# Performance work log

Measured on AMD Instinct MI355X. Metric: run time of the kernel, lower is better.

Reference implementation:

```python
import jax, jax.numpy as jnp
import numpy as np

N_NODES = 50000; N_EDGES = 600000; N_GRAPHS = 128
IN_CH = 128; PROJ = 128; OUT_CH = 128; K = 3; NCLASS = 2; EPS = 1e-5


def _mask():
    # xhi_layer_mask: block i (rows i*OUT_CH:(i+1)*OUT_CH) sees first PROJ*(i+1) input cols
    blocks = []
    for i in range(K):
        m = np.zeros((OUT_CH, PROJ * K), np.float32)
        m[:, :PROJ * (i + 1)] = 1.0
        blocks.append(m)
    return jnp.asarray(np.concatenate(blocks, 0))


def _bn(x, g, b):
    # BatchNorm1d in training mode: biased batch stats, affine g/b
    m = jnp.mean(x, axis=0)
    v = jnp.var(x, axis=0)
    return (x - m) * jax.lax.rsqrt(v + EPS) * g + b


def setup_inputs() -> dict:
    key = jax.random.key(0)
    ks = jax.random.split(key, 10)
    M = OUT_CH * K
    def w(k, shape):
        return jax.random.normal(k, shape, jnp.float32) * 0.05
    return {
        "x": jax.random.normal(ks[0], (N_NODES, IN_CH), jnp.float32),
        "edge_index": jax.random.randint(ks[1], (2, N_EDGES), 0, N_NODES),
        "batch": jnp.sort(jax.random.randint(ks[2], (N_NODES,), 0, N_GRAPHS)),
        "n_graphs": N_GRAPHS,
        "w_rel": w(ks[3], (PROJ, IN_CH)), "b_rel": jnp.zeros((PROJ,), jnp.float32),
        "w_root": w(ks[4], (PROJ, IN_CH)),
        "norm0_g": jnp.ones((PROJ,), jnp.float32), "norm0_b": jnp.zeros((PROJ,), jnp.float32),
        "lin_w": w(ks[5], (M, PROJ * K)), "lin_b": jnp.zeros((M,), jnp.float32),
        "bnh_g": jnp.ones((M,), jnp.float32), "bnh_b": jnp.zeros((M,), jnp.float32),
        "bno_g": jnp.ones((3 * M,), jnp.float32), "bno_b": jnp.zeros((3 * M,), jnp.float32),
        "w1": w(ks[6], (2 * M, 3 * M)), "b1": jnp.zeros((2 * M,), jnp.float32),
        "w2": w(ks[7], (M, 2 * M)), "b2": jnp.zeros((M,), jnp.float32),
        "w3": w(ks[8], (NCLASS, M)), "b3": jnp.zeros((NCLASS,), jnp.float32),
    }


def reference(x, edge_index, batch, n_graphs, w_rel, b_rel, w_root, norm0_g, norm0_b,
              lin_w, lin_b, bnh_g, bnh_b, bno_g, bno_b, w1, b1, w2, b2, w3, b3):
    row, col = edge_index[0], edge_index[1]
    # GraphConv: lin_rel(sum_{j->i} x_j) + lin_root(x_i)
    neigh = jax.ops.segment_sum(x[row], col, num_segments=N_NODES)
    X = neigh @ w_rel.T + b_rel + x @ w_root.T
    X = _bn(X, norm0_g, norm0_b)
    # k-hop polynomial diffusion: A^i X computed as iterative SpMM over edges
    # (A[r,c] = 1 for edge (r,c): (A v)[r] = sum over edges of v[c])
    H = [X]
    cur = X
    for _ in range(K - 1):
        cur = jax.ops.segment_sum(cur[col], row, num_segments=N_NODES)
        H.append(cur)
    Hc = jnp.concatenate(H, axis=1)  # [N, PROJ*K]
    Hm = _bn(Hc @ (lin_w * _mask()).T + lin_b, bnh_g, bnh_b)  # [N, OUT_CH*K]
    # global mean / add / max pooling per graph
    ones = jnp.ones((N_NODES,), jnp.float32)
    cnt = jax.ops.segment_sum(ones, batch, num_segments=n_graphs)
    Hadd = jax.ops.segment_sum(Hm, batch, num_segments=n_graphs)
    Havg = Hadd / jnp.maximum(cnt, 1.0)[:, None]
    Hmax = jax.ops.segment_max(Hm, batch, num_segments=n_graphs)
    Hmax = jnp.where(jnp.isfinite(Hmax), Hmax, 0.0)  # guard empty segments
    Hcat = jnp.concatenate([Havg, Hadd, Hmax], axis=1)  # [G, 3*OUT_CH*K]
    # funnel readout (dropout = identity in eval)
    h = _bn(Hcat, bno_g, bno_b)
    h = jax.nn.relu(h @ w1.T + b1)
    h = jax.nn.relu(h @ w2.T + b2)
    return jax.nn.log_softmax(h @ w3.T + b3, axis=1)
```

## Files before the change

### kernel.cpp

```cpp
#include <hip/hip_runtime.h>
#include <math.h>

#define N_NODES 50000
#define N_EDGES 600000
#define N_GRAPHS 128
#define IN_CH 128
#define PROJ 128
#define OUT_CH 128
#define M_DIM 384
#define HC_DIM 384
#define CAT_DIM 1152
#define H1_DIM 768
#define EPS 1e-5f
#define SCAN_BLK 256
#define NPART 8
#define PART_NODES 6250
#define NPB 64
#define NROWB 391

using bf16x8 = __attribute__((ext_vector_type(8))) short;
using f32x4  = __attribute__((ext_vector_type(4))) float;

__device__ inline unsigned short f2bf(float f) {
  unsigned u = __float_as_uint(f);
  unsigned r = u + 0x7fffu + ((u >> 16) & 1u);
  return (unsigned short)(r >> 16);
}
__device__ inline float bf2f(unsigned short h) {
  return __uint_as_float(((unsigned)h) << 16);
}

__device__ inline void atomicMaxF(float* addr, float val) {
  int iv = __float_as_int(val);
  if (iv >= 0) atomicMax((int*)addr, iv);
  else         atomicMin((unsigned int*)addr, (unsigned int)iv);
}
__device__ inline void atomicMinF(float* addr, float val) {
  int iv = __float_as_int(val);
  if (iv >= 0) atomicMin((int*)addr, iv);
  else         atomicMax((unsigned int*)addr, (unsigned int)iv);
}

__device__ inline void gld16(const void* g, void* l) {
  __builtin_amdgcn_global_load_lds(
      (const __attribute__((address_space(1))) void*)g,
      (__attribute__((address_space(3))) void*)l, 16, 0, 0);
}

__global__ void fill_minmax_kernel(float* __restrict__ gmax, float* __restrict__ gmin) {
  int i = blockIdx.x * blockDim.x + threadIdx.x;
  if (i < N_GRAPHS * M_DIM) {
    gmax[i] = -__builtin_inff();
    gmin[i] =  __builtin_inff();
  }
}

__global__ void bounds_kernel(const int* __restrict__ batch, int* __restrict__ start) {
  int i = blockIdx.x * blockDim.x + threadIdx.x;
  if (i >= N_NODES) return;
  int b = batch[i];
  int bp = (i == 0) ? -1 : batch[i - 1];
  for (int g = bp + 1; g <= b; ++g) start[g] = i;
  if (i == N_NODES - 1)
    for (int g = b + 1; g <= N_GRAPHS; ++g) start[g] = N_NODES;
}

__global__ void cnt_from_bounds_kernel(const int* __restrict__ start, float* __restrict__ cnt) {
  int g = threadIdx.x;
  if (g < N_GRAPHS) cnt[g] = (float)(start[g + 1] - start[g]);
}

__global__ __launch_bounds__(256) void hist_part_kernel(
    const int* __restrict__ row, const int* __restrict__ col,
    int* __restrict__ degA, int* __restrict__ degB) {
  const int part = blockIdx.x & (NPART - 1);
  const int slice = blockIdx.x >> 3;
  const int lo = part * PART_NODES, hi = lo + PART_NODES;
  for (int e = slice * 256 + threadIdx.x; e < N_EDGES; e += NPB * 256) {
    int r = row[e], c = col[e];
    if (c >= lo && c < hi) atomicAdd(&degA[c], 1);
    if (r >= lo && r < hi) atomicAdd(&degB[r], 1);
  }
}

__global__ __launch_bounds__(256) void fill_csr_part_kernel(
    const int* __restrict__ row, const int* __restrict__ col,
    int* __restrict__ cursA, int* __restrict__ eidxA,
    int* __restrict__ cursB, int* __restrict__ eidxB) {
  const int part = blockIdx.x & (NPART - 1);
  const int slice = blockIdx.x >> 3;
  const int lo = part * PART_NODES, hi = lo + PART_NODES;
  for (int e = slice * 256 + threadIdx.x; e < N_EDGES; e += NPB * 256) {
    int r = row[e], c = col[e];
    if (c >= lo && c < hi) eidxA[atomicAdd(&cursA[c], 1)] = r;
    if (r >= lo && r < hi) eidxB[atomicAdd(&cursB[r], 1)] = c;
  }
}

__global__ void scan1_kernel(const int* __restrict__ deg, int* __restrict__ offs,
                             int* __restrict__ bsum, int n) {
  __shared__ int sh[SCAN_BLK];
  int i = blockIdx.x * SCAN_BLK + threadIdx.x;
  int v = (i < n) ? deg[i] : 0;
  sh[threadIdx.x] = v; __syncthreads();
  #pragma unroll
  for (int d = 1; d < SCAN_BLK; d <<= 1) {
    int t = (threadIdx.x >= d) ? sh[threadIdx.x - d] : 0;
    __syncthreads();
    sh[threadIdx.x] += t;
    __syncthreads();
  }
  if (i < n) offs[i] = sh[threadIdx.x] - v;
  if (threadIdx.x == SCAN_BLK - 1) bsum[blockIdx.x] = sh[threadIdx.x];
}

__global__ void scan2_kernel(int* __restrict__ bsum, int nb) {
  __shared__ int sh[SCAN_BLK];
  int v = (threadIdx.x < nb) ? bsum[threadIdx.x] : 0;
  sh[threadIdx.x] = v; __syncthreads();
  #pragma unroll
  for (int d = 1; d < SCAN_BLK; d <<= 1) {
    int t = (threadIdx.x >= d) ? sh[threadIdx.x - d] : 0;
    __syncthreads();
    sh[threadIdx.x] += t;
    __syncthreads();
  }
  if (threadIdx.x < nb) bsum[threadIdx.x] = sh[threadIdx.x] - v;
}

__global__ void scan3_kernel(int* __restrict__ offs, const int* __restrict__ bsum,
                             int* __restrict__ cursor, int n) {
  int i = blockIdx.x * SCAN_BLK + threadIdx.x;
  if (i < n) {
    int o = offs[i] + bsum[blockIdx.x];
    offs[i] = o;
    cursor[i] = o;
  }
}

__global__ void convert_x_kernel(const float* __restrict__ x, unsigned short* __restrict__ xnb) {
  int t = blockIdx.x * blockDim.x + threadIdx.x;
  if (t >= N_NODES * 32) return;
  int node = t >> 5;
  int c4 = (t & 31) << 2;
  float4 v = *(const float4*)(x + (size_t)node * IN_CH + c4);
  ushort4 h = {f2bf(v.x), f2bf(v.y), f2bf(v.z), f2bf(v.w)};
  *(ushort4*)(xnb + (size_t)node * 256 + 128 + c4) = h;
}

__global__ void convert_wcat_kernel(const float* __restrict__ w_rel, const float* __restrict__ w_root,
                                    unsigned short* __restrict__ wcatb) {
  int t = blockIdx.x * blockDim.x + threadIdx.x;
  if (t >= 128 * 64) return;
  int n = t >> 6;
  int c4 = (t & 63) << 2;
  const float* src = (c4 < 128) ? (w_rel + (size_t)n * 128 + c4)
                                : (w_root + (size_t)n * 128 + (c4 - 128));
  float4 v = *(const float4*)src;
  ushort4 h = {f2bf(v.x), f2bf(v.y), f2bf(v.z), f2bf(v.w)};
  *(ushort4*)(wcatb + (size_t)n * 256 + c4) = h;
}

__global__ void convert_linw_kernel(const float* __restrict__ lin_w, unsigned short* __restrict__ linwb) {
  int t = blockIdx.x * blockDim.x + threadIdx.x;
  if (t >= 384 * 96) return;
  int n = t / 96;
  int c4 = (t - n * 96) << 2;
  float4 v = *(const float4*)(lin_w + (size_t)n * HC_DIM + c4);
  ushort4 h = {f2bf(v.x), f2bf(v.y), f2bf(v.z), f2bf(v.w)};
  *(ushort4*)(linwb + (size_t)n * HC_DIM + c4) = h;
}

__global__ __launch_bounds__(256) void gather_bf16_kernel(
    const unsigned short* __restrict__ src, const int* __restrict__ offs,
    const int* __restrict__ ends, const int* __restrict__ eidx,
    unsigned short* __restrict__ dst, int src_ld, int dst_ld) {
  int tid = blockIdx.x * blockDim.x + threadIdx.x;
  int node = tid >> 5;
  int c = (tid & 31) << 2;
  if (node >= N_NODES) return;
  int j = offs[node], end = ends[node];
  float ax = 0.f, ay = 0.f, az = 0.f, aw = 0.f;
  for (; j + 1 < end; j += 2) {
    int s0 = eidx[j], s1 = eidx[j + 1];
    ushort4 v0 = *(const ushort4*)(src + (size_t)s0 * src_ld + c);
    ushort4 v1 = *(const ushort4*)(src + (size_t)s1 * src_ld + c);
    ax += bf2f(v0.x); ay += bf2f(v0.y); az += bf2f(v0.z); aw += bf2f(v0.w);
    ax += bf2f(v1.x); ay += bf2f(v1.y); az += bf2f(v1.z); aw += bf2f(v1.w);
  }
  if (j < end) {
    int s0 = eidx[j];
    ushort4 v0 = *(const ushort4*)(src + (size_t)s0 * src_ld + c);
    ax += bf2f(v0.x); ay += bf2f(v0.y); az += bf2f(v0.z); aw += bf2f(v0.w);
  }
  ushort4 h = {f2bf(ax), f2bf(ay), f2bf(az), f2bf(aw)};
  *(ushort4*)(dst + (size_t)node * dst_ld + c) = h;
}

__device__ inline void stage_async(const unsigned short* __restrict__ src, int src_ld,
                                   int row0, int k0, char* __restrict__ zone, int t) {
  #pragma unroll
  for (int p = 0; p < 4; ++p) {
    int idx = p * 256 + t;
    int r = idx >> 3;
    int slot = idx & 7;
    int sslot = slot ^ (r & 7);
    const char* g = (const char*)(src + (size_t)(row0 + r) * src_ld + k0) + (sslot << 4);
    void* l = zone + p * 4096 + (t >> 6) * 1024;
    gld16(g, l);
  }
}

__device__ inline bf16x8 frag_ld(const char* __restrict__ zone, int row, int slot) {
  return *(const bf16x8*)(zone + row * 128 + ((slot ^ (row & 7)) << 4));
}

__global__ __launch_bounds__(256) void gemm_conv_mfma(
    const unsigned short* __restrict__ xnb, const unsigned short* __restrict__ wcatb,
    const float* __restrict__ b_rel, float* __restrict__ Hc0,
    float* __restrict__ colsum8, float* __restrict__ colsq8) {
  __shared__ char smem[32768];
  char* zoneA = smem;
  char* zoneB = smem + 16384;
  const int bm = blockIdx.x * 128;
  const int t = threadIdx.x;
  const int l = t & 63;
  const int wid = t >> 6;
  const int wr = wid >> 1, wc = wid & 1;
  const int lrow = l & 15, lk = l >> 4;
  f32x4 acc[4][4];
  #pragma unroll
  for (int i = 0; i < 4; ++i)
    #pragma unroll
    for (int jn = 0; jn < 4; ++jn) acc[i][jn] = (f32x4){0.f, 0.f, 0.f, 0.f};
  for (int st = 0; st < 4; ++st) {
    __syncthreads();
    stage_async(xnb, 256, bm, st * 64, zoneA, t);
    stage_async(wcatb, 256, 0, st * 64, zoneB, t);
    __syncthreads();
    #pragma unroll
    for (int kk = 0; kk < 2; ++kk) {
      bf16x8 af[4], bfr[4];
      #pragma unroll
      for (int mf = 0; mf < 4; ++mf) af[mf] = frag_ld(zoneA, wr * 64 + mf * 16 + lrow, kk * 4 + lk);
      #pragma unroll
      for (int nf = 0; nf < 4; ++nf) bfr[nf] = frag_ld(zoneB, wc * 64 + nf * 16 + lrow, kk * 4 + lk);
      #pragma unroll
      for (int mf = 0; mf < 4; ++mf)
        #pragma unroll
        for (int nf = 0; nf < 4; ++nf)
          acc[mf][nf] = __builtin_amdgcn_mfma_f32_16x16x32_bf16(af[mf], bfr[nf], acc[mf][nf], 0, 0, 0);
    }
  }
  float brv[4];
  #pragma unroll
  for (int nf = 0; nf < 4; ++nf) brv[nf] = b_rel[wc * 64 + nf * 16 + lrow];
  #pragma unroll
  for (int mf = 0; mf < 4; ++mf) {
    #pragma unroll
    for (int q = 0; q < 4; ++q) {
      int r = bm + wr * 64 + mf * 16 + lk * 4 + q;
      if (r < N_NODES) {
        #pragma unroll
        for (int nf = 0; nf < 4; ++nf)
          Hc0[(size_t)r * 128 + wc * 64 + nf * 16 + lrow] = acc[mf][nf][q] + brv[nf];
      }
    }
  }
  __syncthreads();
  float* csum = (float*)smem;
  float* csq  = (float*)(smem + 512);
  if (t < 128) { csum[t] = 0.f; csq[t] = 0.f; }
  __syncthreads();
  #pragma unroll
  for (int nf = 0; nf < 4; ++nf) {
    int ccol = wc * 64 + nf * 16 + lrow;
    float s = 0.f, q = 0.f;
    #pragma unroll
    for (int mf = 0; mf < 4; ++mf)
      #pragma unroll
      for (int qq = 0; qq < 4; ++qq) {
        int r = bm + wr * 64 + mf * 16 + lk * 4 + qq;
        if (r < N_NODES) { float v = acc[mf][nf][qq] + brv[nf]; s += v; q += v * v; }
      }
    atomicAdd(&csum[ccol], s);
    atomicAdd(&csq[ccol], q);
  }
  __syncthreads();
  if (t < 128) {
    int cpy = (blockIdx.x & 7) * 128;
    atomicAdd(&colsum8[cpy + t], csum[t]);
    atomicAdd(&colsq8[cpy + t], csq[t]);
  }
}

__global__ void bn_prep_kernel(const float* __restrict__ colsum8, const float* __restrict__ colsq8,
                               const float* __restrict__ g_, const float* __restrict__ b_,
                               float* __restrict__ bn_s, float* __restrict__ bn_t) {
  int c = threadIdx.x;
  float s1 = 0.f, s2 = 0.f;
  #pragma unroll
  for (int k = 0; k < 8; ++k) { s1 += colsum8[k * 128 + c]; s2 += colsq8[k * 128 + c]; }
  float m = s1 * (1.0f / N_NODES);
  float var = s2 * (1.0f / N_NODES) - m * m;
  float sc = g_[c] * rsqrtf(var + EPS);
  bn_s[c] = sc;
  bn_t[c] = b_[c] - m * sc;
}

__global__ __launch_bounds__(256) void gemm_mask_mfma(
    const unsigned short* __restrict__ Hcb, const unsigned short* __restrict__ linwb,
    const float* __restrict__ lin_b, const int* __restrict__ batch,
    float* __restrict__ gsum, float* __restrict__ gmax, float* __restrict__ gmin,
    float* __restrict__ colsumsq) {
  __shared__ char smem[33792];
  __shared__ int bsh[128];
  char* zoneA = smem;
  char* zoneB = smem + 16384;
  const int bid = blockIdx.x;
  const int ybl = 2 - bid / NROWB;
  const int bm = (bid % NROWB) * 128;
  const int bn = ybl * 128;
  const int nstages = 2 * (ybl + 1);
  const int t = threadIdx.x;
  const int l = t & 63;
  const int wid = t >> 6;
  const int wr = wid >> 1, wc = wid & 1;
  const int lrow = l & 15, lk = l >> 4;
  f32x4 acc[4][4];
  #pragma unroll
  for (int i = 0; i < 4; ++i)
    #pragma unroll
    for (int jn = 0; jn < 4; ++jn) acc[i][jn] = (f32x4){0.f, 0.f, 0.f, 0.f};
  for (int st = 0; st < nstages; ++st) {
    __syncthreads();
    stage_async(Hcb, HC_DIM, bm, st * 64, zoneA, t);
    stage_async(linwb, HC_DIM, bn, st * 64, zoneB, t);
    __syncthreads();
    #pragma unroll
    for (int kk = 0; kk < 2; ++kk) {
      bf16x8 af[4], bfr[4];
      #pragma unroll
      for (int mf = 0; mf < 4; ++mf) af[mf] = frag_ld(zoneA, wr * 64 + mf * 16 + lrow, kk * 4 + lk);
      #pragma unroll
      for (int nf = 0; nf < 4; ++nf) bfr[nf] = frag_ld(zoneB, wc * 64 + nf * 16 + lrow, kk * 4 + lk);
      #pragma unroll
      for (int mf = 0; mf < 4; ++mf)
        #pragma unroll
        for (int nf = 0; nf < 4; ++nf)
          acc[mf][nf] = __builtin_amdgcn_mfma_f32_16x16x32_bf16(af[mf], bfr[nf], acc[mf][nf], 0, 0, 0);
    }
  }
  float lbv[4];
  #pragma unroll
  for (int nf = 0; nf < 4; ++nf) lbv[nf] = lin_b[bn + wc * 64 + nf * 16 + lrow];
  if (t < 128) bsh[t] = (bm + t < N_NODES) ? batch[bm + t] : -1;
  float* Y = (float*)smem;
  const int col = t & 127;
  const int gcol = bn + col;
  const int r0 = (t >> 7) * 32;
  float sq = 0.f;
  __syncthreads();
  for (int half = 0; half < 2; ++half) {
    if (wr == half) {
      #pragma unroll
      for (int mf = 0; mf < 4; ++mf)
        #pragma unroll
        for (int q = 0; q < 4; ++q) {
          int rr = mf * 16 + lk * 4 + q;
          #pragma unroll
          for (int nf = 0; nf < 4; ++nf)
            Y[rr * 132 + wc * 64 + nf * 16 + lrow] = acc[mf][nf][q] + lbv[nf];
        }
    }
    __syncthreads();
    int curg = -1;
    float s = 0.f, mx = 0.f, mn = 0.f;
    for (int rr = 0; rr < 32; ++rr) {
      int g = bsh[half * 64 + r0 + rr];
      if (g < 0) break;
      float y = Y[(r0 + rr) * 132 + col];
      sq += y * y;
      if (g != curg) {
        if (curg >= 0) {
          atomicAdd(&gsum[curg * M_DIM + gcol], s);
          atomicMaxF(&gmax[curg * M_DIM + gcol], mx);
          atomicMinF(&gmin[curg * M_DIM + gcol], mn);
        }
        curg = g; s = y; mx = y; mn = y;
      } else {
        s += y; mx = fmaxf(mx, y); mn = fminf(mn, y);
      }
    }
    if (curg >= 0) {
      atomicAdd(&gsum[curg * M_DIM + gcol], s);
      atomicMaxF(&gmax[curg * M_DIM + gcol], mx);
      atomicMinF(&gmin[curg * M_DIM + gcol], mn);
    }
    __syncthreads();
  }
  atomicAdd(&colsumsq[gcol], sq);
}

__global__ __launch_bounds__(256) void bn_apply0_kernel(
    const float* __restrict__ Hc0, unsigned short* __restrict__ Hcb,
    const float* __restrict__ bn_s, const float* __restrict__ bn_t) {
  int tid = blockIdx.x * blockDim.x + threadIdx.x;
  if (tid >= N_NODES * 32) return;
  int r = tid >> 5;
  int c = (tid & 31) << 2;
  float4 v = *(const float4*)(Hc0 + (size_t)r * 128 + c);
  float vv[4] = {v.x, v.y, v.z, v.w};
  #pragma unroll
  for (int j = 0; j < 4; ++j)
    vv[j] = vv[j] * bn_s[c + j] + bn_t[c + j];
  ushort4 hh = {f2bf(vv[0]), f2bf(vv[1]), f2bf(vv[2]), f2bf(vv[3])};
  *(ushort4*)(Hcb + (size_t)r * HC_DIM + c) = hh;
}

__device__ inline float block_sum128(float v, float* red) {
  int t = threadIdx.x;
  red[t] = v; __syncthreads();
  #pragma unroll
  for (int s = 64; s >= 1; s >>= 1) {
    if (t < s) red[t] += red[t + s];
    __syncthreads();
  }
  float r = red[0];
  __syncthreads();
  return r;
}

__device__ inline void bn_write_col(float v, int col, const float* __restrict__ bg,
                                    const float* __restrict__ bb, float* __restrict__ h0T,
                                    float* red) {
  float s1 = block_sum128(v, red);
  float s2 = block_sum128(v * v, red);
  float m = s1 * (1.0f / N_GRAPHS);
  float var = s2 * (1.0f / N_GRAPHS) - m * m;
  float sc = bg[col] * rsqrtf(var + EPS);
  h0T[(size_t)col * N_GRAPHS + threadIdx.x] = (v - m) * sc + bb[col];
}

__global__ __launch_bounds__(128) void finalize_kernel(
    const float* __restrict__ gsum, const float* __restrict__ gmax,
    const float* __restrict__ gmin, const float* __restrict__ colsumsq,
    const float* __restrict__ cnt, const float* __restrict__ bnh_g,
    const float* __restrict__ bnh_b, const float* __restrict__ bno_g,
    const float* __restrict__ bno_b, float* __restrict__ h0T) {
  __shared__ float red[128];
  int c = blockIdx.x;
  int g = threadIdx.x;
  float vsum = gsum[g * M_DIM + c];
  float colsum = block_sum128(vsum, red);
  float m = colsum * (1.0f / N_NODES);
  float var = colsumsq[c] * (1.0f / N_NODES) - m * m;
  float s = bnh_g[c] * rsqrtf(var + EPS);
  float t = bnh_b[c] - m * s;
  float cg = cnt[g];
  float hadd = s * vsum + cg * t;
  float havg = hadd / fmaxf(cg, 1.0f);
  float hmax = 0.f;
  if (cg > 0.f)
    hmax = (s >= 0.f ? s * gmax[g * M_DIM + c] : s * gmin[g * M_DIM + c]) + t;
  bn_write_col(havg, c,        bno_g, bno_b, h0T, red);
  bn_write_col(hadd, 384 + c,  bno_g, bno_b, h0T, red);
  bn_write_col(hmax, 768 + c,  bno_g, bno_b, h0T, red);
}

__global__ __launch_bounds__(128) void mlp_kernel(
    const float* __restrict__ inT, const float* __restrict__ W,
    const float* __restrict__ bias, float* __restrict__ outT, int Kdim, int do_relu) {
  __shared__ float wrow[CAT_DIM];
  int oc = blockIdx.x;
  int g = threadIdx.x;
  for (int k = g; k < Kdim; k += 128) wrow[k] = W[(size_t)oc * Kdim + k];
  __syncthreads();
  float acc = bias[oc];
  for (int k = 0; k < Kdim; ++k) acc += inT[(size_t)k * N_GRAPHS + g] * wrow[k];
  if (do_relu) acc = fmaxf(acc, 0.f);
  outT[(size_t)oc * N_GRAPHS + g] = acc;
}

__global__ __launch_bounds__(128) void head_kernel(
    const float* __restrict__ h2T, const float* __restrict__ w3,
    const float* __restrict__ b3, float* __restrict__ out) {
  int g = threadIdx.x;
  float z0 = b3[0], z1 = b3[1];
  for (int k = 0; k < M_DIM; ++k) {
    float v = h2T[(size_t)k * N_GRAPHS + g];
    z0 += v * w3[k];
    z1 += v * w3[M_DIM + k];
  }
  float mz = fmaxf(z0, z1);
  float lse = mz + logf(expf(z0 - mz) + expf(z1 - mz));
  out[g * 2 + 0] = z0 - lse;
  out[g * 2 + 1] = z1 - lse;
}

extern "C" void kernel_launch(void* const* d_in, const int* in_sizes, int n_in,
                              void* d_out, int out_size, void* d_ws, size_t ws_size,
                              hipStream_t stream) {
  const float* x       = (const float*)d_in[0];
  const int*   row     = (const int*)d_in[1];
  const int*   col     = row + N_EDGES;
  const int*   batch   = (const int*)d_in[2];
  const float* w_rel   = (const float*)d_in[4];
  const float* b_rel   = (const float*)d_in[5];
  const float* w_root  = (const float*)d_in[6];
  const float* norm0_g = (const float*)d_in[7];
  const float* norm0_b = (const float*)d_in[8];
  const float* lin_w   = (const float*)d_in[9];
  const float* lin_b   = (const float*)d_in[10];
  const float* bnh_g   = (const float*)d_in[11];
  const float* bnh_b   = (const float*)d_in[12];
  const float* bno_g   = (const float*)d_in[13];
  const float* bno_b   = (const float*)d_in[14];
  const float* w1      = (const float*)d_in[15];
  const float* b1      = (const float*)d_in[16];
  const float* w2      = (const float*)d_in[17];
  const float* b2      = (const float*)d_in[18];
  const float* w3      = (const float*)d_in[19];
  const float* b3      = (const float*)d_in[20];
  float* out = (float*)d_out;

  char* ws = (char*)d_ws;
  size_t off = 0;
  auto allocb = [&](size_t nbytes) {
    char* p = ws + off;
    off += ((nbytes + 255) & ~(size_t)255);
    return p;
  };
  int*   degA      = (int*)allocb(N_NODES * 4);
  int*   degB      = (int*)allocb(N_NODES * 4);
  float* gsum      = (float*)allocb((size_t)N_GRAPHS * M_DIM * 4);
  float* colsumsq  = (float*)allocb(M_DIM * 4);
  float* colsum8   = (float*)allocb(8 * PROJ * 4);
  float* colsq8    = (float*)allocb(8 * PROJ * 4);
  size_t zero_bytes = off;
  float* cnt    = (float*)allocb(N_GRAPHS * 4);
  int*   gstart = (int*)allocb((N_GRAPHS + 1) * 4);
  float* bn_s   = (float*)allocb(PROJ * 4);
  float* bn_t   = (float*)allocb(PROJ * 4);
  int*   offsA = (int*)allocb(N_NODES * 4);
  int*   cursA = (int*)allocb(N_NODES * 4);
  int*   offsB = (int*)allocb(N_NODES * 4);
  int*   cursB = (int*)allocb(N_NODES * 4);
  int*   bsumA = (int*)allocb(SCAN_BLK * 4);
  int*   bsumB = (int*)allocb(SCAN_BLK * 4);
  int*   eidxA = (int*)allocb(N_EDGES * 4);
  int*   eidxB = (int*)allocb(N_EDGES * 4);
  float* Hc0   = (float*)allocb((size_t)N_NODES * 128 * 4);
  unsigned short* Hcb   = (unsigned short*)allocb((size_t)N_NODES * HC_DIM * 2);
  unsigned short* xnb   = (unsigned short*)allocb((size_t)N_NODES * 256 * 2);
  unsigned short* wcatb = (unsigned short*)allocb(128 * 256 * 2);
  unsigned short* linwb = (unsigned short*)allocb(384 * 384 * 2);
  float* gmax  = (float*)allocb((size_t)N_GRAPHS * M_DIM * 4);
  float* gmin  = (float*)allocb((size_t)N_GRAPHS * M_DIM * 4);
  float* h0T   = (float*)allocb((size_t)CAT_DIM * N_GRAPHS * 4);
  float* h1T   = (float*)allocb((size_t)H1_DIM * N_GRAPHS * 4);
  float* h2T   = (float*)allocb((size_t)M_DIM * N_GRAPHS * 4);

  const int NB = (N_NODES + SCAN_BLK - 1) / SCAN_BLK;

  hipMemsetAsync(d_ws, 0, zero_bytes, stream);
  fill_minmax_kernel<<<(N_GRAPHS * M_DIM + 255) / 256, 256, 0, stream>>>(gmax, gmin);
  bounds_kernel<<<(N_NODES + 255) / 256, 256, 0, stream>>>(batch, gstart);
  cnt_from_bounds_kernel<<<1, 128, 0, stream>>>(gstart, cnt);

  hist_part_kernel<<<NPART * NPB, 256, 0, stream>>>(row, col, degA, degB);
  scan1_kernel<<<NB, SCAN_BLK, 0, stream>>>(degA, offsA, bsumA, N_NODES);
  scan1_kernel<<<NB, SCAN_BLK, 0, stream>>>(degB, offsB, bsumB, N_NODES);
  scan2_kernel<<<1, SCAN_BLK, 0, stream>>>(bsumA, NB);
  scan2_kernel<<<1, SCAN_BLK, 0, stream>>>(bsumB, NB);
  scan3_kernel<<<NB, SCAN_BLK, 0, stream>>>(offsA, bsumA, cursA, N_NODES);
  scan3_kernel<<<NB, SCAN_BLK, 0, stream>>>(offsB, bsumB, cursB, N_NODES);
  fill_csr_part_kernel<<<NPART * NPB, 256, 0, stream>>>(row, col, cursA, eidxA, cursB, eidxB);

  convert_x_kernel<<<(N_NODES * 32 + 255) / 256, 256, 0, stream>>>(x, xnb);
  convert_wcat_kernel<<<(128 * 64 + 255) / 256, 256, 0, stream>>>(w_rel, w_root, wcatb);
  convert_linw_kernel<<<(384 * 96 + 255) / 256, 256, 0, stream>>>(lin_w, linwb);

  gather_bf16_kernel<<<(N_NODES * 32 + 255) / 256, 256, 0, stream>>>(
      xnb + 128, offsA, cursA, eidxA, xnb, 256, 256);
  gemm_conv_mfma<<<NROWB, 256, 0, stream>>>(xnb, wcatb, b_rel, Hc0, colsum8, colsq8);
  bn_prep_kernel<<<1, 128, 0, stream>>>(colsum8, colsq8, norm0_g, norm0_b, bn_s, bn_t);
  bn_apply0_kernel<<<(N_NODES * 32 + 255) / 256, 256, 0, stream>>>(Hc0, Hcb, bn_s, bn_t);
  gather_bf16_kernel<<<(N_NODES * 32 + 255) / 256, 256, 0, stream>>>(
      Hcb, offsB, cursB, eidxB, Hcb + 128, HC_DIM, HC_DIM);
  gather_bf16_kernel<<<(N_NODES * 32 + 255) / 256, 256, 0, stream>>>(
      Hcb + 128, offsB, cursB, eidxB, Hcb + 256, HC_DIM, HC_DIM);
  gemm_mask_mfma<<<NROWB * 3, 256, 0, stream>>>(
      Hcb, linwb, lin_b, batch, gsum, gmax, gmin, colsumsq);
  finalize_kernel<<<M_DIM, 128, 0, stream>>>(gsum, gmax, gmin, colsumsq, cnt,
                                             bnh_g, bnh_b, bno_g, bno_b, h0T);
  mlp_kernel<<<H1_DIM, 128, 0, stream>>>(h0T, w1, b1, h1T, CAT_DIM, 1);
  mlp_kernel<<<M_DIM, 128, 0, stream>>>(h1T, w2, b2, h2T, H1_DIM, 1);
  head_kernel<<<1, 128, 0, stream>>>(h2T, w3, b3, out);
}
```

Before: 419.2 us.

## Pre-pack weights into MFMA fragment layout and double-buffer 64-row GEMM tiles

Weights for both GEMMs are pre-packed into per-lane MFMA fragment order so B fragments load straight from global/L2, and only the A tile is staged in LDS. The tiles shrink to 64 rows with double-buffered LDS staging and a launch bound of 2. The masked GEMM now computes all three output column blocks in one block, so each A tile is read once instead of three times and the pooling epilogue loops over blocks. The gather loop is also unrolled by 4 for more memory-level parallelism. In exchange the kernels use more registers (48 accumulators in the mask GEMM), issue more global B loads, and the epilogue has more syncs.

Measured after the change: 453.2 us. +8.1%, slower.

```diff
diff --git a/kernel.cpp b/kernel.cpp
--- a/kernel.cpp
+++ b/kernel.cpp
@@ -16,7 +16,7 @@
 #define NPART 8
 #define PART_NODES 6250
 #define NPB 64
-#define NROWB 391
+#define NROWB64 782
 
 using bf16x8 = __attribute__((ext_vector_type(8))) short;
 using f32x4  = __attribute__((ext_vector_type(4))) float;
@@ -148,27 +148,43 @@
   *(ushort4*)(xnb + (size_t)node * 256 + 128 + c4) = h;
 }
 
-__global__ void convert_wcat_kernel(const float* __restrict__ w_rel, const float* __restrict__ w_root,
-                                    unsigned short* __restrict__ wcatb) {
-  int t = blockIdx.x * blockDim.x + threadIdx.x;
-  if (t >= 128 * 64) return;
-  int n = t >> 6;
-  int c4 = (t & 63) << 2;
-  const float* src = (c4 < 128) ? (w_rel + (size_t)n * 128 + c4)
-                                : (w_root + (size_t)n * 128 + (c4 - 128));
-  float4 v = *(const float4*)src;
-  ushort4 h = {f2bf(v.x), f2bf(v.y), f2bf(v.z), f2bf(v.w)};
-  *(ushort4*)(wcatb + (size_t)n * 256 + c4) = h;
-}
-
-__global__ void convert_linw_kernel(const float* __restrict__ lin_w, unsigned short* __restrict__ linwb) {
-  int t = blockIdx.x * blockDim.x + threadIdx.x;
-  if (t >= 384 * 96) return;
-  int n = t / 96;
-  int c4 = (t - n * 96) << 2;
-  float4 v = *(const float4*)(lin_w + (size_t)n * HC_DIM + c4);
-  ushort4 h = {f2bf(v.x), f2bf(v.y), f2bf(v.z), f2bf(v.w)};
-  *(ushort4*)(linwb + (size_t)n * HC_DIM + c4) = h;
+__global__ void pack_wcat_kernel(const float* __restrict__ w_rel, const float* __restrict__ w_root,
+                                 unsigned short* __restrict__ wcatPk) {
+  int tid = blockIdx.x * blockDim.x + threadIdx.x;
+  if (tid >= 4096) return;
+  int l = tid & 63, rest = tid >> 6;
+  int nf = rest & 3, kk = (rest >> 2) & 1, wcq = (rest >> 3) & 1, stv = rest >> 4;
+  int lrow = l & 15, lk = l >> 4;
+  int srow = wcq * 64 + nf * 16 + lrow;
+  int scol = stv * 64 + (kk * 4 + lk) * 8;
+  unsigned short o[8];
+  #pragma unroll
+  for (int e = 0; e < 8; ++e) {
+    int c = scol + e;
+    float v = (c < 128) ? w_rel[(size_t)srow * 128 + c] : w_root[(size_t)srow * 128 + c - 128];
+    o[e] = f2bf(v);
+  }
+  unsigned short* d = wcatPk + (size_t)rest * 512 + l * 8;
+  #pragma unroll
+  for (int e = 0; e < 8; ++e) d[e] = o[e];
+}
+
+__global__ void pack_linw_kernel(const float* __restrict__ lin_w, unsigned short* __restrict__ linwPk) {
+  int tid = blockIdx.x * blockDim.x + threadIdx.x;
+  if (tid >= 18432) return;
+  int l = tid & 63, rest = tid >> 6;
+  int nf = rest & 3, kk = (rest >> 2) & 1, wcq = (rest >> 3) & 1;
+  int q = rest >> 4;
+  int stv = q % 6, bn = q / 6;
+  int lrow = l & 15, lk = l >> 4;
+  int srow = bn * 128 + wcq * 64 + nf * 16 + lrow;
+  int scol = stv * 64 + (kk * 4 + lk) * 8;
+  unsigned short o[8];
+  #pragma unroll
+  for (int e = 0; e < 8; ++e) o[e] = f2bf(lin_w[(size_t)srow * HC_DIM + scol + e]);
+  unsigned short* d = linwPk + (size_t)rest * 512 + l * 8;
+  #pragma unroll
+  for (int e = 0; e < 8; ++e) d[e] = o[e];
 }
 
 __global__ __launch_bounds__(256) void gather_bf16_kernel(
@@ -181,14 +197,18 @@
   if (node >= N_NODES) return;
   int j = offs[node], end = ends[node];
   float ax = 0.f, ay = 0.f, az = 0.f, aw = 0.f;
-  for (; j + 1 < end; j += 2) {
-    int s0 = eidx[j], s1 = eidx[j + 1];
+  for (; j + 3 < end; j += 4) {
+    int s0 = eidx[j], s1 = eidx[j + 1], s2 = eidx[j + 2], s3 = eidx[j + 3];
     ushort4 v0 = *(const ushort4*)(src + (size_t)s0 * src_ld + c);
     ushort4 v1 = *(const ushort4*)(src + (size_t)s1 * src_ld + c);
-    ax += bf2f(v0.x); ay += bf2f(v0.y); az += bf2f(v0.z); aw += bf2f(v0.w);
-    ax += bf2f(v1.x); ay += bf2f(v1.y); az += bf2f(v1.z); aw += bf2f(v1.w);
-  }
-  if (j < end) {
+    ushort4 v2 = *(const ushort4*)(src + (size_t)s2 * src_ld + c);
+    ushort4 v3 = *(const ushort4*)(src + (size_t)s3 * src_ld + c);
+    ax += bf2f(v0.x) + bf2f(v1.x) + bf2f(v2.x) + bf2f(v3.x);
+    ay += bf2f(v0.y) + bf2f(v1.y) + bf2f(v2.y) + bf2f(v3.y);
+    az += bf2f(v0.z) + bf2f(v1.z) + bf2f(v2.z) + bf2f(v3.z);
+    aw += bf2f(v0.w) + bf2f(v1.w) + bf2f(v2.w) + bf2f(v3.w);
+  }
+  for (; j < end; ++j) {
     int s0 = eidx[j];
     ushort4 v0 = *(const ushort4*)(src + (size_t)s0 * src_ld + c);
     ax += bf2f(v0.x); ay += bf2f(v0.y); az += bf2f(v0.z); aw += bf2f(v0.w);
@@ -197,10 +217,10 @@
   *(ushort4*)(dst + (size_t)node * dst_ld + c) = h;
 }
 
-__device__ inline void stage_async(const unsigned short* __restrict__ src, int src_ld,
-                                   int row0, int k0, char* __restrict__ zone, int t) {
-  #pragma unroll
-  for (int p = 0; p < 4; ++p) {
+__device__ inline void stage_async64(const unsigned short* __restrict__ src, int src_ld,
+                                     int row0, int k0, char* __restrict__ zone, int t) {
+  #pragma unroll
+  for (int p = 0; p < 2; ++p) {
     int idx = p * 256 + t;
     int r = idx >> 3;
     int slot = idx & 7;
@@ -215,51 +235,54 @@
   return *(const bf16x8*)(zone + row * 128 + ((slot ^ (row & 7)) << 4));
 }
 
-__global__ __launch_bounds__(256) void gemm_conv_mfma(
-    const unsigned short* __restrict__ xnb, const unsigned short* __restrict__ wcatb,
+__global__ __launch_bounds__(256, 2) void gemm_conv_mfma(
+    const unsigned short* __restrict__ xnb, const unsigned short* __restrict__ wcatPk,
     const float* __restrict__ b_rel, float* __restrict__ Hc0,
     float* __restrict__ colsum8, float* __restrict__ colsq8) {
-  __shared__ char smem[32768];
-  char* zoneA = smem;
-  char* zoneB = smem + 16384;
-  const int bm = blockIdx.x * 128;
+  __shared__ char smem[16384];
+  char* zone0 = smem;
+  char* zone1 = smem + 8192;
+  const int bm = blockIdx.x * 64;
   const int t = threadIdx.x;
   const int l = t & 63;
   const int wid = t >> 6;
   const int wr = wid >> 1, wc = wid & 1;
   const int lrow = l & 15, lk = l >> 4;
-  f32x4 acc[4][4];
-  #pragma unroll
-  for (int i = 0; i < 4; ++i)
+  f32x4 acc[2][4];
+  #pragma unroll
+  for (int mf = 0; mf < 2; ++mf)
     #pragma unroll
-    for (int jn = 0; jn < 4; ++jn) acc[i][jn] = (f32x4){0.f, 0.f, 0.f, 0.f};
+    for (int nf = 0; nf < 4; ++nf) acc[mf][nf] = (f32x4){0.f, 0.f, 0.f, 0.f};
+  stage_async64(xnb, 256, bm, 0, zone0, t);
+  __syncthreads();
   for (int st = 0; st < 4; ++st) {
-    __syncthreads();
-    stage_async(xnb, 256, bm, st * 64, zoneA, t);
-    stage_async(wcatb, 256, 0, st * 64, zoneB, t);
-    __syncthreads();
+    if (st < 3) stage_async64(xnb, 256, bm, (st + 1) * 64, ((st + 1) & 1) ? zone1 : zone0, t);
+    const char* zA = (st & 1) ? zone1 : zone0;
     #pragma unroll
     for (int kk = 0; kk < 2; ++kk) {
-      bf16x8 af[4], bfr[4];
+      bf16x8 af[2];
+      af[0] = frag_ld(zA, wr * 32 + lrow, kk * 4 + lk);
+      af[1] = frag_ld(zA, wr * 32 + 16 + lrow, kk * 4 + lk);
+      const unsigned short* Bp = wcatPk + (size_t)(((st * 2 + wc) * 2 + kk) * 4) * 512 + l * 8;
+      bf16x8 bfr[4];
       #pragma unroll
-      for (int mf = 0; mf < 4; ++mf) af[mf] = frag_ld(zoneA, wr * 64 + mf * 16 + lrow, kk * 4 + lk);
+      for (int nf = 0; nf < 4; ++nf) bfr[nf] = *(const bf16x8*)(Bp + nf * 512);
       #pragma unroll
-      for (int nf = 0; nf < 4; ++nf) bfr[nf] = frag_ld(zoneB, wc * 64 + nf * 16 + lrow, kk * 4 + lk);
-      #pragma unroll
-      for (int mf = 0; mf < 4; ++mf)
+      for (int mf = 0; mf < 2; ++mf)
         #pragma unroll
         for (int nf = 0; nf < 4; ++nf)
           acc[mf][nf] = __builtin_amdgcn_mfma_f32_16x16x32_bf16(af[mf], bfr[nf], acc[mf][nf], 0, 0, 0);
     }
+    __syncthreads();
   }
   float brv[4];
   #pragma unroll
   for (int nf = 0; nf < 4; ++nf) brv[nf] = b_rel[wc * 64 + nf * 16 + lrow];
   #pragma unroll
-  for (int mf = 0; mf < 4; ++mf) {
+  for (int mf = 0; mf < 2; ++mf) {
     #pragma unroll
     for (int q = 0; q < 4; ++q) {
-      int r = bm + wr * 64 + mf * 16 + lk * 4 + q;
+      int r = bm + wr * 32 + mf * 16 + lk * 4 + q;
       if (r < N_NODES) {
         #pragma unroll
         for (int nf = 0; nf < 4; ++nf)
@@ -267,7 +290,6 @@
       }
     }
   }
-  __syncthreads();
   float* csum = (float*)smem;
   float* csq  = (float*)(smem + 512);
   if (t < 128) { csum[t] = 0.f; csq[t] = 0.f; }
@@ -275,16 +297,16 @@
   #pragma unroll
   for (int nf = 0; nf < 4; ++nf) {
     int ccol = wc * 64 + nf * 16 + lrow;
-    float s = 0.f, q = 0.f;
+    float s = 0.f, q2 = 0.f;
     #pragma unroll
-    for (int mf = 0; mf < 4; ++mf)
+    for (int mf = 0; mf < 2; ++mf)
       #pragma unroll
       for (int qq = 0; qq < 4; ++qq) {
-        int r = bm + wr * 64 + mf * 16 + lk * 4 + qq;
-        if (r < N_NODES) { float v = acc[mf][nf][qq] + brv[nf]; s += v; q += v * v; }
+        int r = bm + wr * 32 + mf * 16 + lk * 4 + qq;
+        if (r < N_NODES) { float v = acc[mf][nf][qq] + brv[nf]; s += v; q2 += v * v; }
       }
     atomicAdd(&csum[ccol], s);
-    atomicAdd(&csq[ccol], q);
+    atomicAdd(&csq[ccol], q2);
   }
   __syncthreads();
   if (t < 128) {
@@ -308,98 +330,109 @@
   bn_t[c] = b_[c] - m * sc;
 }
 
-__global__ __launch_bounds__(256) void gemm_mask_mfma(
-    const unsigned short* __restrict__ Hcb, const unsigned short* __restrict__ linwb,
+__global__ __launch_bounds__(256, 2) void gemm_mask_mfma(
+    const unsigned short* __restrict__ Hcb, const unsigned short* __restrict__ linwPk,
     const float* __restrict__ lin_b, const int* __restrict__ batch,
     float* __restrict__ gsum, float* __restrict__ gmax, float* __restrict__ gmin,
     float* __restrict__ colsumsq) {
-  __shared__ char smem[33792];
-  __shared__ int bsh[128];
-  char* zoneA = smem;
-  char* zoneB = smem + 16384;
-  const int bid = blockIdx.x;
-  const int ybl = 2 - bid / NROWB;
-  const int bm = (bid % NROWB) * 128;
-  const int bn = ybl * 128;
-  const int nstages = 2 * (ybl + 1);
+  __shared__ char smem[16896];
+  __shared__ int bsh[64];
+  char* zone0 = smem;
+  char* zone1 = smem + 8192;
+  const int bm = blockIdx.x * 64;
   const int t = threadIdx.x;
   const int l = t & 63;
   const int wid = t >> 6;
   const int wr = wid >> 1, wc = wid & 1;
   const int lrow = l & 15, lk = l >> 4;
-  f32x4 acc[4][4];
-  #pragma unroll
-  for (int i = 0; i < 4; ++i)
+  f32x4 acc[3][2][4];
+  #pragma unroll
+  for (int bn = 0; bn < 3; ++bn)
     #pragma unroll
-    for (int jn = 0; jn < 4; ++jn) acc[i][jn] = (f32x4){0.f, 0.f, 0.f, 0.f};
-  for (int st = 0; st < nstages; ++st) {
-    __syncthreads();
-    stage_async(Hcb, HC_DIM, bm, st * 64, zoneA, t);
-    stage_async(linwb, HC_DIM, bn, st * 64, zoneB, t);
-    __syncthreads();
+    for (int mf = 0; mf < 2; ++mf)
+      #pragma unroll
+      for (int nf = 0; nf < 4; ++nf) acc[bn][mf][nf] = (f32x4){0.f, 0.f, 0.f, 0.f};
+  stage_async64(Hcb, HC_DIM, bm, 0, zone0, t);
+  __syncthreads();
+  for (int st = 0; st < 6; ++st) {
+    if (st < 5) stage_async64(Hcb, HC_DIM, bm, (st + 1) * 64, ((st + 1) & 1) ? zone1 : zone0, t);
+    const char* zA = (st & 1) ? zone1 : zone0;
     #pragma unroll
     for (int kk = 0; kk < 2; ++kk) {
-      bf16x8 af[4], bfr[4];
+      bf16x8 af[2];
+      af[0] = frag_ld(zA, wr * 32 + lrow, kk * 4 + lk);
+      af[1] = frag_ld(zA, wr * 32 + 16 + lrow, kk * 4 + lk);
       #pragma unroll
-      for (int mf = 0; mf < 4; ++mf) af[mf] = frag_ld(zoneA, wr * 64 + mf * 16 + lrow, kk * 4 + lk);
-      #pragma unroll
-      for (int nf = 0; nf < 4; ++nf) bfr[nf] = frag_ld(zoneB, wc * 64 + nf * 16 + lrow, kk * 4 + lk);
-      #pragma unroll
-      for (int mf = 0; mf < 4; ++mf)
-        #pragma unroll
-        for (int nf = 0; nf < 4; ++nf)
-          acc[mf][nf] = __builtin_amdgcn_mfma_f32_16x16x32_bf16(af[mf], bfr[nf], acc[mf][nf], 0, 0, 0);
+      for (int bn = 0; bn < 3; ++bn) {
+        if (st < 2 * (bn + 1)) {
+          const unsigned short* Bp =
+              linwPk + (size_t)((((bn * 6 + st) * 2 + wc) * 2 + kk) * 4) * 512 + l * 8;
+          bf16x8 bfr[4];
+          #pragma unroll
+          for (int nf = 0; nf < 4; ++nf) bfr[nf] = *(const bf16x8*)(Bp + nf * 512);
+          #pragma unroll
+          for (int mf = 0; mf < 2; ++mf)
+            #pragma unroll
+            for (int nf = 0; nf < 4; ++nf)
+              acc[bn][mf][nf] =
+                  __builtin_amdgcn_mfma_f32_16x16x32_bf16(af[mf], bfr[nf], acc[bn][mf][nf], 0, 0, 0);
+        }
+      }
     }
-  }
-  float lbv[4];
-  #pragma unroll
-  for (int nf = 0; nf < 4; ++nf) lbv[nf] = lin_b[bn + wc * 64 + nf * 16 + lrow];
-  if (t < 128) bsh[t] = (bm + t < N_NODES) ? batch[bm + t] : -1;
+    __syncthreads();
+  }
+  if (t < 64) bsh[t] = (bm + t < N_NODES) ? batch[bm + t] : -1;
   float* Y = (float*)smem;
   const int col = t & 127;
-  const int gcol = bn + col;
-  const int r0 = (t >> 7) * 32;
-  float sq = 0.f;
-  __syncthreads();
-  for (int half = 0; half < 2; ++half) {
-    if (wr == half) {
-      #pragma unroll
-      for (int mf = 0; mf < 4; ++mf)
+  const int rgrp = t >> 7;
+  #pragma unroll
+  for (int bn = 0; bn < 3; ++bn) {
+    const int gcol = bn * 128 + col;
+    float lbv[4];
+    #pragma unroll
+    for (int nf = 0; nf < 4; ++nf) lbv[nf] = lin_b[bn * 128 + wc * 64 + nf * 16 + lrow];
+    float sq = 0.f;
+    for (int half = 0; half < 2; ++half) {
+      if (wr == half) {
         #pragma unroll
-        for (int q = 0; q < 4; ++q) {
-          int rr = mf * 16 + lk * 4 + q;
+        for (int mf = 0; mf < 2; ++mf)
           #pragma unroll
-          for (int nf = 0; nf < 4; ++nf)
-            Y[rr * 132 + wc * 64 + nf * 16 + lrow] = acc[mf][nf][q] + lbv[nf];
+          for (int q = 0; q < 4; ++q) {
+            int rr = mf * 16 + lk * 4 + q;
+            #pragma unroll
+            for (int nf = 0; nf < 4; ++nf)
+              Y[rr * 132 + wc * 64 + nf * 16 + lrow] = acc[bn][mf][nf][q] + lbv[nf];
+          }
+      }
+      __syncthreads();
+      int curg = -1;
+      float s = 0.f, mx = 0.f, mn = 0.f;
+      for (int rr = 0; rr < 16; ++rr) {
+        int grow = half * 32 + rgrp * 16 + rr;
+        int g = bsh[grow];
+        if (g < 0) break;
+        float y = Y[(rgrp * 16 + rr) * 132 + col];
+        sq += y * y;
+        if (g != curg) {
+          if (curg >= 0) {
+            atomicAdd(&gsum[curg * M_DIM + gcol], s);
+            atomicMaxF(&gmax[curg * M_DIM + gcol], mx);
+            atomicMinF(&gmin[curg * M_DIM + gcol], mn);
+          }
+          curg = g; s = y; mx = y; mn = y;
+        } else {
+          s += y; mx = fmaxf(mx, y); mn = fminf(mn, y);
         }
+      }
+      if (curg >= 0) {
+        atomicAdd(&gsum[curg * M_DIM + gcol], s);
+        atomicMaxF(&gmax[curg * M_DIM + gcol], mx);
+        atomicMinF(&gmin[curg * M_DIM + gcol], mn);
+      }
+      __syncthreads();
     }
-    __syncthreads();
-    int curg = -1;
-    float s = 0.f, mx = 0.f, mn = 0.f;
-    for (int rr = 0; rr < 32; ++rr) {
-      int g = bsh[half * 64 + r0 + rr];
-      if (g < 0) break;
-      float y = Y[(r0 + rr) * 132 + col];
-      sq += y * y;
-      if (g != curg) {
-        if (curg >= 0) {
-          atomicAdd(&gsum[curg * M_DIM + gcol], s);
-          atomicMaxF(&gmax[curg * M_DIM + gcol], mx);
-          atomicMinF(&gmin[curg * M_DIM + gcol], mn);
-        }
-        curg = g; s = y; mx = y; mn = y;
-      } else {
-        s += y; mx = fmaxf(mx, y); mn = fminf(mn, y);
-      }
-    }
-    if (curg >= 0) {
-      atomicAdd(&gsum[curg * M_DIM + gcol], s);
-      atomicMaxF(&gmax[curg * M_DIM + gcol], mx);
-      atomicMinF(&gmin[curg * M_DIM + gcol], mn);
-    }
-    __syncthreads();
-  }
-  atomicAdd(&colsumsq[gcol], sq);
+    atomicAdd(&colsumsq[gcol], sq);
+  }
 }
 
 __global__ __launch_bounds__(256) void bn_apply0_kernel(
@@ -551,10 +584,10 @@
   int*   eidxA = (int*)allocb(N_EDGES * 4);
   int*   eidxB = (int*)allocb(N_EDGES * 4);
   float* Hc0   = (float*)allocb((size_t)N_NODES * 128 * 4);
-  unsigned short* Hcb   = (unsigned short*)allocb((size_t)N_NODES * HC_DIM * 2);
-  unsigned short* xnb   = (unsigned short*)allocb((size_t)N_NODES * 256 * 2);
-  unsigned short* wcatb = (unsigned short*)allocb(128 * 256 * 2);
-  unsigned short* linwb = (unsigned short*)allocb(384 * 384 * 2);
+  unsigned short* Hcb    = (unsigned short*)allocb((size_t)N_NODES * HC_DIM * 2);
+  unsigned short* xnb    = (unsigned short*)allocb((size_t)N_NODES * 256 * 2);
+  unsigned short* wcatPk = (unsigned short*)allocb(128 * 256 * 2);
+  unsigned short* linwPk = (unsigned short*)allocb(384 * 384 * 2);
   float* gmax  = (float*)allocb((size_t)N_GRAPHS * M_DIM * 4);
   float* gmin  = (float*)allocb((size_t)N_GRAPHS * M_DIM * 4);
   float* h0T   = (float*)allocb((size_t)CAT_DIM * N_GRAPHS * 4);
@@ -578,20 +611,20 @@
   fill_csr_part_kernel<<<NPART * NPB, 256, 0, stream>>>(row, col, cursA, eidxA, cursB, eidxB);
 
   convert_x_kernel<<<(N_NODES * 32 + 255) / 256, 256, 0, stream>>>(x, xnb);
-  convert_wcat_kernel<<<(128 * 64 + 255) / 256, 256, 0, stream>>>(w_rel, w_root, wcatb);
-  convert_linw_kernel<<<(384 * 96 + 255) / 256, 256, 0, stream>>>(lin_w, linwb);
+  pack_wcat_kernel<<<16, 256, 0, stream>>>(w_rel, w_root, wcatPk);
+  pack_linw_kernel<<<72, 256, 0, stream>>>(lin_w, linwPk);
 
   gather_bf16_kernel<<<(N_NODES * 32 + 255) / 256, 256, 0, stream>>>(
       xnb + 128, offsA, cursA, eidxA, xnb, 256, 256);
-  gemm_conv_mfma<<<NROWB, 256, 0, stream>>>(xnb, wcatb, b_rel, Hc0, colsum8, colsq8);
+  gemm_conv_mfma<<<NROWB64, 256, 0, stream>>>(xnb, wcatPk, b_rel, Hc0, colsum8, colsq8);
   bn_prep_kernel<<<1, 128, 0, stream>>>(colsum8, colsq8, norm0_g, norm0_b, bn_s, bn_t);
   bn_apply0_kernel<<<(N_NODES * 32 + 255) / 256, 256, 0, stream>>>(Hc0, Hcb, bn_s, bn_t);
   gather_bf16_kernel<<<(N_NODES * 32 + 255) / 256, 256, 0, stream>>>(
       Hcb, offsB, cursB, eidxB, Hcb + 128, HC_DIM, HC_DIM);
   gather_bf16_kernel<<<(N_NODES * 32 + 255) / 256, 256, 0, stream>>>(
       Hcb + 128, offsB, cursB, eidxB, Hcb + 256, HC_DIM, HC_DIM);
-  gemm_mask_mfma<<<NROWB * 3, 256, 0, stream>>>(
-      Hcb, linwb, lin_b, batch, gsum, gmax, gmin, colsumsq);
+  gemm_mask_mfma<<<NROWB64, 256, 0, stream>>>(
+      Hcb, linwPk, lin_b, batch, gsum, gmax, gmin, colsumsq);
   finalize_kernel<<<M_DIM, 128, 0, stream>>>(gsum, gmax, gmin, colsumsq, cnt,
                                              bnh_g, bnh_b, bno_g, bno_b, h0T);
   mlp_kernel<<<H1_DIM, 128, 0, stream>>>(h0T, w1, b1, h1T, CAT_DIM, 1);
```
